# Performance work log

Measured on AMD Instinct MI355X. Metric: run time of the kernel, lower is better.

The kernel has to match this reference:

```python
import jax, jax.numpy as jnp
import numpy as np

CLIP_TEMPERATURE = 1.0


def setup_inputs() -> dict:
    key = jax.random.key(0)
    k1, k2 = jax.random.split(key)
    N, D = 16384, 256
    x = jax.random.normal(k1, (N, D), dtype=jnp.float32)
    y = jax.random.normal(k2, (N, D), dtype=jnp.float32)
    return {"x": x, "y": y}


def reference(x, y):
    # logits[i, j] = <x_i, y_j> / T ; labels are the diagonal (i-th text matches i-th image)
    logits = jnp.einsum('id,jd->ij', x, y) / CLIP_TEMPERATURE  # [N, N]
    N = logits.shape[0]
    diag_idx = jnp.arange(N)
    # CrossEntropy(logits, labels=arange) == -mean(diag(log_softmax(logits, axis=1)))
    lsm_row = jax.nn.log_softmax(logits, axis=1)  # image -> text
    lsm_col = jax.nn.log_softmax(logits, axis=0)  # text  -> image (== log_softmax(logits.T, axis=1).T)
    loss_row = -jnp.mean(lsm_row[diag_idx, diag_idx])
    loss_col = -jnp.mean(lsm_col[diag_idx, diag_idx])
    return (loss_row + loss_col) * 0.5
```

## Files before the change

### kernel.cpp

```cpp
#include <hip/hip_runtime.h>
#include <hip/hip_bf16.h>

#define NN 16384
#define DD 256
#define PANEL 256
#define JCOLS 128
#define BKT 64
#define NT 4
#define NJ 16
#define THREADS 512
#define A_BYTES (PANEL * DD * 2)
#define B_BYTES (JCOLS * BKT * 2)
#define LDS_TOTAL (A_BYTES + 2 * B_BYTES)
#define SHIFT_C 64.0f
#define LOG2E 1.4426950408889634f

typedef __attribute__((ext_vector_type(4))) float f32x4;
typedef __attribute__((ext_vector_type(8))) short bf16x8;

#if __has_builtin(__builtin_amdgcn_exp2f)
#define EXP2F(x) __builtin_amdgcn_exp2f(x)
#else
#define EXP2F(x) exp2f(x)
#endif

__device__ __forceinline__ unsigned pkbf(float a, float b) {
  float2 t; t.x = a; t.y = b;
  __hip_bfloat162 h = __float22bfloat162_rn(t);
  union { __hip_bfloat162 h; unsigned u; } cv;
  cv.h = h;
  return cv.u;
}

__device__ __forceinline__ float rowsum16_dpp(float v) {
  union { float f; int i; } x, t;
  x.f = v;
  t.i = __builtin_amdgcn_update_dpp(0, x.i, 0x111, 0xf, 0xf, true); x.f += t.f;
  t.i = __builtin_amdgcn_update_dpp(0, x.i, 0x112, 0xf, 0xf, true); x.f += t.f;
  t.i = __builtin_amdgcn_update_dpp(0, x.i, 0x114, 0xf, 0xf, true); x.f += t.f;
  t.i = __builtin_amdgcn_update_dpp(0, x.i, 0x118, 0xf, 0xf, true); x.f += t.f;
  return x.f;
}

__global__ __launch_bounds__(256) void cvt_kernel(
    const float* __restrict__ X, const float* __restrict__ Y,
    unsigned short* __restrict__ Xb, unsigned short* __restrict__ Yb) {
  const int groups_per_arr = NN * DD / 8;
  int g = blockIdx.x * 256 + threadIdx.x;
  const float* src;
  unsigned short* dst;
  if (g < groups_per_arr) { src = X; dst = Xb; }
  else { src = Y; dst = Yb; g -= groups_per_arr; }
  float4 a = ((const float4*)src)[(size_t)g * 2];
  float4 b = ((const float4*)src)[(size_t)g * 2 + 1];
  uint4 p = { pkbf(a.x, a.y), pkbf(a.z, a.w), pkbf(b.x, b.y), pkbf(b.z, b.w) };
  ((uint4*)dst)[g] = p;
}

__global__ __launch_bounds__(THREADS, 2) void clip_gemm(
    const unsigned short* __restrict__ Xb, const unsigned short* __restrict__ Yb,
    float* __restrict__ rowsum, float* __restrict__ colsum,
    float* __restrict__ diagsum) {
  extern __shared__ unsigned char sm[];

  const int tid = threadIdx.x;
  const int bid = blockIdx.x;
  const int xcd = bid & 7;
  const int panel = xcd * 8 + ((bid >> 3) & 7);
  const int colgroup = bid >> 6;
  const int rowbase = panel * PANEL;
  const int colbase = colgroup * (NJ * JCOLS);

  const unsigned short* xb = Xb + (size_t)rowbase * DD;
  const unsigned short* ybg = Yb + (size_t)colbase * DD;

  const int wid = tid >> 6, lane = tid & 63;
  const int wm = wid >> 1, wn = wid & 1;
  const int lm = lane & 15, lk = lane >> 4;

#pragma unroll
  for (int p = 0; p < 16; ++p) {
    const int s = p * 512 + tid;
    const int row = s >> 5;
    const int g = (s & 31) ^ (row & 7);
    __builtin_amdgcn_global_load_lds(
        (const __attribute__((address_space(1))) unsigned*)(xb + row * DD + g * 8),
        (__attribute__((address_space(3))) unsigned*)(sm + s * 16), 16, 0, 0);
  }

  int bsrc[2], bdst[2];
#pragma unroll
  for (int p = 0; p < 2; ++p) {
    const int s = p * 512 + tid;
    const int row = s >> 3;
    const int g = (s & 7) ^ (row & 7);
    bsrc[p] = row * DD + g * 8;
    bdst[p] = A_BYTES + s * 16;
  }

#define GLOADB(jn, tn, buf)                                                    \
  {                                                                            \
    _Pragma("unroll")                                                          \
    for (int p = 0; p < 2; ++p)                                                \
      __builtin_amdgcn_global_load_lds(                                        \
          (const __attribute__((address_space(1))) unsigned*)(ybg + (size_t)(jn) * (JCOLS * DD) + bsrc[p] + (tn) * BKT), \
          (__attribute__((address_space(3))) unsigned*)(sm + (buf) * B_BYTES + bdst[p]), \
          16, 0, 0);                                                           \
  }

#define RDA(m, t, kh)                                                          \
  (*(const bf16x8*)(sm + (wm * 64 + (m) * 16 + lm) * (DD * 2) +                \
                    ((((t) * 8 + (kh) * 4 + lk) ^ (lm & 7)) << 4)))
#define RDB(nf, kh, buf)                                                       \
  (*(const bf16x8*)(sm + A_BYTES + (buf) * B_BYTES +                           \
                    (wn * 64 + (nf) * 16 + lm) * (BKT * 2) +                   \
                    ((((kh) * 4 + lk) ^ (lm & 7)) << 4)))

  f32x4 acc[4][4] = {};
  float rowacc[4][4];
#pragma unroll
  for (int m = 0; m < 4; ++m)
#pragma unroll
    for (int r = 0; r < 4; ++r) rowacc[m][r] = 0.f;
  float dsum = 0.f;
  const float negC = -(SHIFT_C * LOG2E);

  GLOADB(0, 0, 0);

  for (int j = 0; j < NJ; ++j) {
#pragma unroll
    for (int t = 0; t < NT; ++t) {
      __syncthreads();
      if (t < NT - 1) { GLOADB(j, t + 1, (t + 1) & 1); }
      else if (j < NJ - 1) { GLOADB(j + 1, 0, 0); }
      const int buf = t & 1;
      bf16x8 a0, b0[4];
#pragma unroll
      for (int kh = 0; kh < 2; ++kh) {
#pragma unroll
        for (int nf = 0; nf < 4; ++nf) b0[nf] = RDB(nf, kh, buf);
#pragma unroll
        for (int m = 0; m < 4; ++m) {
          a0 = RDA(m, t, kh);
#pragma unroll
          for (int nf = 0; nf < 4; ++nf)
            acc[m][nf] = __builtin_amdgcn_mfma_f32_16x16x32_bf16(a0, b0[nf], acc[m][nf], 0, 0, 0);
        }
      }
    }

    const int jc0 = colbase + j * JCOLS;
    float colacc[4] = {0.f, 0.f, 0.f, 0.f};
#pragma unroll
    for (int m = 0; m < 4; ++m)
#pragma unroll
      for (int nf = 0; nf < 4; ++nf)
#pragma unroll
        for (int r = 0; r < 4; ++r) {
          float e = EXP2F(__builtin_fmaf(acc[m][nf][r], LOG2E, negC));
          rowacc[m][r] += e;
          colacc[nf] += e;
        }
    if (jc0 < rowbase + PANEL && jc0 + JCOLS > rowbase) {
#pragma unroll
      for (int m = 0; m < 4; ++m)
#pragma unroll
        for (int nf = 0; nf < 4; ++nf)
#pragma unroll
          for (int r = 0; r < 4; ++r) {
            const int gr = rowbase + wm * 64 + m * 16 + lk * 4 + r;
            const int gc = jc0 + wn * 64 + nf * 16 + lm;
            if (gr == gc) dsum += acc[m][nf][r];
          }
    }
#pragma unroll
    for (int nf = 0; nf < 4; ++nf) {
      float v = colacc[nf];
      v += __shfl_xor(v, 16);
      v += __shfl_xor(v, 32);
      if (lk == 0)
        atomicAdd(&colsum[jc0 + wn * 64 + nf * 16 + lm], v);
    }
    const f32x4 z4 = {0.f, 0.f, 0.f, 0.f};
#pragma unroll
    for (int m = 0; m < 4; ++m)
#pragma unroll
      for (int nf = 0; nf < 4; ++nf) acc[m][nf] = z4;
  }
#undef GLOADB
#undef RDA
#undef RDB

  {
    float d = dsum;
    d += __shfl_xor(d, 1);
    d += __shfl_xor(d, 2);
    d += __shfl_xor(d, 4);
    d += __shfl_xor(d, 8);
    d += __shfl_xor(d, 16);
    d += __shfl_xor(d, 32);
    if (lane == 0 && d != 0.f) atomicAdd(diagsum, d);
  }
#pragma unroll
  for (int m = 0; m < 4; ++m)
#pragma unroll
    for (int r = 0; r < 4; ++r) {
      float v = rowsum16_dpp(rowacc[m][r]);
      if (lm == 15)
        atomicAdd(&rowsum[rowbase + wm * 64 + m * 16 + lk * 4 + r], v);
    }
}

__global__ __launch_bounds__(256) void clip_main_fb(
    const float* __restrict__ X, const float* __restrict__ Y,
    float* __restrict__ rowsum, float* __restrict__ colsum,
    float* __restrict__ diagsum) {
  __shared__ __align__(16) unsigned char smem[2 * 128 * 64 * 2];
  unsigned char* smA = smem;
  unsigned char* smB = smem + 128 * 64 * 2;

  const int tid = threadIdx.x;
  const int bid = blockIdx.x;
  const int swz = (bid & 7) * 2048 + (bid >> 3);
  const int brow = swz >> 7;
  const int bcol = swz & 127;

  const float* xb = X + (size_t)brow * 128 * DD;
  const float* yb = Y + (size_t)bcol * 128 * DD;

  const int wid = tid >> 6, lane = tid & 63;
  const int wm = wid >> 1, wn = wid & 1;
  const int lm = lane & 15, lk = lane >> 4;

  f32x4 acc[4][4] = {};

  for (int ks = 0; ks < 4; ++ks) {
    const int kbase = ks * 64;
    if (ks) __syncthreads();
#pragma unroll
    for (int i = 0; i < 4; ++i) {
      const int c = tid + i * 256;
      const int row = c >> 3, slot = c & 7;
      const int boff = row * 128 + ((slot << 4) ^ ((row & 7) << 4));
      const float* ga = xb + row * DD + kbase + (slot << 3);
      float4 a0 = *(const float4*)ga;
      float4 a1 = *(const float4*)(ga + 4);
      uint4 pa = { pkbf(a0.x, a0.y), pkbf(a0.z, a0.w),
                   pkbf(a1.x, a1.y), pkbf(a1.z, a1.w) };
      *(uint4*)(smA + boff) = pa;
      const float* gb = yb + row * DD + kbase + (slot << 3);
      float4 b0 = *(const float4*)gb;
      float4 b1 = *(const float4*)(gb + 4);
      uint4 pb = { pkbf(b0.x, b0.y), pkbf(b0.z, b0.w),
                   pkbf(b1.x, b1.y), pkbf(b1.z, b1.w) };
      *(uint4*)(smB + boff) = pb;
    }
    __syncthreads();

#pragma unroll
    for (int kk = 0; kk < 2; ++kk) {
      const int kboff = kk * 64 + lk * 16;
      bf16x8 a[4], b[4];
#pragma unroll
      for (int m = 0; m < 4; ++m) {
        const int row = wm * 64 + m * 16 + lm;
        a[m] = *(const bf16x8*)(smA + row * 128 + (kboff ^ ((row & 7) << 4)));
      }
#pragma unroll
      for (int n = 0; n < 4; ++n) {
        const int row = wn * 64 + n * 16 + lm;
        b[n] = *(const bf16x8*)(smB + row * 128 + (kboff ^ ((row & 7) << 4)));
      }
#pragma unroll
      for (int m = 0; m < 4; ++m)
#pragma unroll
        for (int n = 0; n < 4; ++n)
          acc[m][n] = __builtin_amdgcn_mfma_f32_16x16x32_bf16(a[m], b[n], acc[m][n], 0, 0, 0);
    }
  }

  float rowacc[4][4];
  float colacc[4];
#pragma unroll
  for (int m = 0; m < 4; ++m)
#pragma unroll
    for (int r = 0; r < 4; ++r) rowacc[m][r] = 0.f;
#pragma unroll
  for (int n = 0; n < 4; ++n) colacc[n] = 0.f;

  const float negC = -(SHIFT_C * LOG2E);
#pragma unroll
  for (int m = 0; m < 4; ++m)
#pragma unroll
    for (int n = 0; n < 4; ++n)
#pragma unroll
      for (int r = 0; r < 4; ++r) {
        float e = EXP2F(__builtin_fmaf(acc[m][n][r], LOG2E, negC));
        rowacc[m][r] += e;
        colacc[n] += e;
      }

  if (brow == bcol && wm == wn) {
    float dsum = 0.f;
#pragma unroll
    for (int m = 0; m < 4; ++m)
#pragma unroll
      for (int n = 0; n < 4; ++n)
#pragma unroll
        for (int r = 0; r < 4; ++r) {
          const int rr = m * 16 + lk * 4 + r;
          const int cc = n * 16 + lm;
          if (rr == cc) dsum += acc[m][n][r];
        }
    dsum += __shfl_xor(dsum, 1);
    dsum += __shfl_xor(dsum, 2);
    dsum += __shfl_xor(dsum, 4);
    dsum += __shfl_xor(dsum, 8);
    dsum += __shfl_xor(dsum, 16);
    dsum += __shfl_xor(dsum, 32);
    if (lane == 0) atomicAdd(diagsum, dsum);
  }

#pragma unroll
  for (int m = 0; m < 4; ++m)
#pragma unroll
    for (int r = 0; r < 4; ++r) {
      float v = rowsum16_dpp(rowacc[m][r]);
      if (lm == 15)
        atomicAdd(&rowsum[brow * 128 + wm * 64 + m * 16 + lk * 4 + r], v);
    }
#pragma unroll
  for (int n = 0; n < 4; ++n) {
    float v = colacc[n];
    v += __shfl_xor(v, 16);
    v += __shfl_xor(v, 32);
    if (lk == 0)
      atomicAdd(&colsum[bcol * 128 + wn * 64 + n * 16 + lm], v);
  }
}

__global__ __launch_bounds__(256) void clip_stats(
    const float* __restrict__ rowsum, const float* __restrict__ colsum,
    float* __restrict__ partial) {
  __shared__ float sdata[4];
  const int i = blockIdx.x * 256 + threadIdx.x;
  float s = logf(rowsum[i]) + logf(colsum[i]);
  s += __shfl_xor(s, 1);
  s += __shfl_xor(s, 2);
  s += __shfl_xor(s, 4);
  s += __shfl_xor(s, 8);
  s += __shfl_xor(s, 16);
  s += __shfl_xor(s, 32);
  const int lane = threadIdx.x & 63, wv = threadIdx.x >> 6;
  if (lane == 0) sdata[wv] = s;
  __syncthreads();
  if (threadIdx.x == 0)
    atomicAdd(partial, sdata[0] + sdata[1] + sdata[2] + sdata[3]);
}

__global__ void clip_out(const float* __restrict__ partial,
                         const float* __restrict__ diagsum,
                         float* __restrict__ out) {
  if (threadIdx.x == 0)
    out[0] = (float)((double)SHIFT_C + (double)partial[0] * 0.5 / (double)NN
                     - (double)diagsum[0] / (double)NN);
}

extern "C" void kernel_launch(void* const* d_in, const int* in_sizes, int n_in,
                              void* d_out, int out_size, void* d_ws, size_t ws_size,
                              hipStream_t stream) {
  const float* X = (const float*)d_in[0];
  const float* Y = (const float*)d_in[1];

  const size_t bf16_bytes = (size_t)2 * NN * DD * sizeof(unsigned short);
  const size_t stats_bytes = (size_t)(2 * NN + 2) * sizeof(float);

  if (ws_size >= bf16_bytes + stats_bytes) {
    unsigned short* Xb = (unsigned short*)d_ws;
    unsigned short* Yb = Xb + (size_t)NN * DD;
    float* rowsum = (float*)((unsigned char*)d_ws + bf16_bytes);
    float* colsum = rowsum + NN;
    float* diagsum = colsum + NN;
    float* partial = diagsum + 1;

    hipMemsetAsync(rowsum, 0, stats_bytes, stream);
    cvt_kernel<<<dim3(2 * NN * DD / 8 / 256), dim3(256), 0, stream>>>(X, Y, Xb, Yb);
    clip_gemm<<<dim3(512), dim3(THREADS), LDS_TOTAL, stream>>>(
        Xb, Yb, rowsum, colsum, diagsum);
    clip_stats<<<dim3(NN / 256), dim3(256), 0, stream>>>(rowsum, colsum, partial);
    clip_out<<<dim3(1), dim3(64), 0, stream>>>(partial, diagsum, (float*)d_out);
  } else {
    float* rowsum = (float*)d_ws;
    float* colsum = rowsum + NN;
    float* diagsum = colsum + NN;
    float* partial = diagsum + 1;
    hipMemsetAsync(d_ws, 0, stats_bytes, stream);
    clip_main_fb<<<dim3((NN / 128) * (NN / 128)), dim3(256), 0, stream>>>(
        X, Y, rowsum, colsum, diagsum);
    clip_stats<<<dim3(NN / 256), dim3(256), 0, stream>>>(rowsum, colsum, partial);
    clip_out<<<dim3(1), dim3(64), 0, stream>>>(partial, diagsum, (float*)d_out);
  }
}
```

Baseline: 210.2 us.

## Load B operands directly into registers and remap blocks so XCDs share column groups

Drops the LDS double buffer for the Y tile and its per-step __syncthreads; each wave instead fetches its B fragments straight from global memory into registers, prefetched one k-step ahead. Block indexing is also remapped so consecutive blocks (spread across XCDs) take different column groups of the same row panel. The goal is to remove barrier stalls and LDS traffic for B. The cost is redundant global/L2 reads, since the waves that share a column (wm varies) each load the same B data, plus more registers held for the prefetch.

```diff
diff --git a/kernel.cpp b/kernel.cpp
--- a/kernel.cpp
+++ b/kernel.cpp
@@ -5,13 +5,10 @@
 #define DD 256
 #define PANEL 256
 #define JCOLS 128
-#define BKT 64
 #define NT 4
 #define NJ 16
 #define THREADS 512
 #define A_BYTES (PANEL * DD * 2)
-#define B_BYTES (JCOLS * BKT * 2)
-#define LDS_TOTAL (A_BYTES + 2 * B_BYTES)
 #define SHIFT_C 64.0f
 #define LOG2E 1.4426950408889634f
 
@@ -65,9 +62,8 @@
 
   const int tid = threadIdx.x;
   const int bid = blockIdx.x;
-  const int xcd = bid & 7;
-  const int panel = xcd * 8 + ((bid >> 3) & 7);
-  const int colgroup = bid >> 6;
+  const int colgroup = bid & 7;
+  const int panel = bid >> 3;
   const int rowbase = panel * PANEL;
   const int colbase = colgroup * (NJ * JCOLS);
 
@@ -87,34 +83,22 @@
         (const __attribute__((address_space(1))) unsigned*)(xb + row * DD + g * 8),
         (__attribute__((address_space(3))) unsigned*)(sm + s * 16), 16, 0, 0);
   }
-
-  int bsrc[2], bdst[2];
-#pragma unroll
-  for (int p = 0; p < 2; ++p) {
-    const int s = p * 512 + tid;
-    const int row = s >> 3;
-    const int g = (s & 7) ^ (row & 7);
-    bsrc[p] = row * DD + g * 8;
-    bdst[p] = A_BYTES + s * 16;
-  }
-
-#define GLOADB(jn, tn, buf)                                                    \
-  {                                                                            \
-    _Pragma("unroll")                                                          \
-    for (int p = 0; p < 2; ++p)                                                \
-      __builtin_amdgcn_global_load_lds(                                        \
-          (const __attribute__((address_space(1))) unsigned*)(ybg + (size_t)(jn) * (JCOLS * DD) + bsrc[p] + (tn) * BKT), \
-          (__attribute__((address_space(3))) unsigned*)(sm + (buf) * B_BYTES + bdst[p]), \
-          16, 0, 0);                                                           \
-  }
+  __syncthreads();
 
 #define RDA(m, t, kh)                                                          \
   (*(const bf16x8*)(sm + (wm * 64 + (m) * 16 + lm) * (DD * 2) +                \
                     ((((t) * 8 + (kh) * 4 + lk) ^ (lm & 7)) << 4)))
-#define RDB(nf, kh, buf)                                                       \
-  (*(const bf16x8*)(sm + A_BYTES + (buf) * B_BYTES +                           \
-                    (wn * 64 + (nf) * 16 + lm) * (BKT * 2) +                   \
-                    ((((kh) * 4 + lk) ^ (lm & 7)) << 4)))
+
+  const unsigned short* ybl = ybg + (size_t)(wn * 64 + lm) * DD + lk * 8;
+
+#define LOADB(dst, yj, t)                                                      \
+  {                                                                            \
+    _Pragma("unroll")                                                          \
+    for (int nf = 0; nf < 4; ++nf) {                                           \
+      dst[0][nf] = *(const bf16x8*)((yj) + nf * 16 * DD + (t) * 64);           \
+      dst[1][nf] = *(const bf16x8*)((yj) + nf * 16 * DD + (t) * 64 + 32);      \
+    }                                                                          \
+  }
 
   f32x4 acc[4][4] = {};
   float rowacc[4][4];
@@ -125,26 +109,25 @@
   float dsum = 0.f;
   const float negC = -(SHIFT_C * LOG2E);
 
-  GLOADB(0, 0, 0);
+  bf16x8 breg[2][2][4];
+
+  LOADB(breg[0], ybl, 0);
 
   for (int j = 0; j < NJ; ++j) {
+    const unsigned short* yj = ybl + (size_t)j * (JCOLS * DD);
 #pragma unroll
     for (int t = 0; t < NT; ++t) {
-      __syncthreads();
-      if (t < NT - 1) { GLOADB(j, t + 1, (t + 1) & 1); }
-      else if (j < NJ - 1) { GLOADB(j + 1, 0, 0); }
-      const int buf = t & 1;
-      bf16x8 a0, b0[4];
+      if (t < NT - 1) { LOADB(breg[(t + 1) & 1], yj, t + 1); }
+      else if (j < NJ - 1) { LOADB(breg[0], yj + (JCOLS * DD), 0); }
 #pragma unroll
       for (int kh = 0; kh < 2; ++kh) {
 #pragma unroll
-        for (int nf = 0; nf < 4; ++nf) b0[nf] = RDB(nf, kh, buf);
-#pragma unroll
         for (int m = 0; m < 4; ++m) {
-          a0 = RDA(m, t, kh);
+          const bf16x8 a0 = RDA(m, t, kh);
 #pragma unroll
           for (int nf = 0; nf < 4; ++nf)
-            acc[m][nf] = __builtin_amdgcn_mfma_f32_16x16x32_bf16(a0, b0[nf], acc[m][nf], 0, 0, 0);
+            acc[m][nf] = __builtin_amdgcn_mfma_f32_16x16x32_bf16(
+                a0, breg[t & 1][kh][nf], acc[m][nf], 0, 0, 0);
         }
       }
     }
@@ -187,9 +170,8 @@
 #pragma unroll
       for (int nf = 0; nf < 4; ++nf) acc[m][nf] = z4;
   }
-#undef GLOADB
+#undef LOADB
 #undef RDA
-#undef RDB
 
   {
     float d = dsum;
@@ -385,7 +367,7 @@
 
     hipMemsetAsync(rowsum, 0, stats_bytes, stream);
     cvt_kernel<<<dim3(2 * NN * DD / 8 / 256), dim3(256), 0, stream>>>(X, Y, Xb, Yb);
-    clip_gemm<<<dim3(512), dim3(THREADS), LDS_TOTAL, stream>>>(
+    clip_gemm<<<dim3(512), dim3(THREADS), A_BYTES, stream>>>(
         Xb, Yb, rowsum, colsum, diagsum);
     clip_stats<<<dim3(NN / 256), dim3(256), 0, stream>>>(rowsum, colsum, partial);
     clip_out<<<dim3(1), dim3(64), 0, stream>>>(partial, diagsum, (float*)d_out);
```

Result: slower. 386.8 us (+84.0%).

## Shrink GEMM tiles to 128-row panels with 256 threads and static LDS

Applied to the files above, without the earlier changes.

Each block now handles 128 rows instead of 256, using 4 waves instead of 8. The B k-step drops from 64 to 32, so there are 8 k-tiles with a matching swizzle. The grid doubles to 1024 blocks with a simpler panel/column-group mapping that drops the XCD-aware assignment, and LDS becomes a static 80KB array so more blocks can be resident per CU. The cost is half the X-panel reuse, twice as many reads of Y across panels, and more barriers per output tile.

```diff
diff --git a/kernel.cpp b/kernel.cpp
--- a/kernel.cpp
+++ b/kernel.cpp
@@ -3,15 +3,14 @@
 
 #define NN 16384
 #define DD 256
-#define PANEL 256
+#define PANEL 128
 #define JCOLS 128
-#define BKT 64
-#define NT 4
+#define BK 32
+#define NT 8
 #define NJ 16
-#define THREADS 512
+#define THREADS 256
 #define A_BYTES (PANEL * DD * 2)
-#define B_BYTES (JCOLS * BKT * 2)
-#define LDS_TOTAL (A_BYTES + 2 * B_BYTES)
+#define B_BYTES (JCOLS * BK * 2)
 #define SHIFT_C 64.0f
 #define LOG2E 1.4426950408889634f
 
@@ -61,13 +60,12 @@
     const unsigned short* __restrict__ Xb, const unsigned short* __restrict__ Yb,
     float* __restrict__ rowsum, float* __restrict__ colsum,
     float* __restrict__ diagsum) {
-  extern __shared__ unsigned char sm[];
+  __shared__ __align__(16) unsigned char sm[A_BYTES + 2 * B_BYTES];
 
   const int tid = threadIdx.x;
   const int bid = blockIdx.x;
-  const int xcd = bid & 7;
-  const int panel = xcd * 8 + ((bid >> 3) & 7);
-  const int colgroup = bid >> 6;
+  const int colgroup = bid & 7;
+  const int panel = bid >> 3;
   const int rowbase = panel * PANEL;
   const int colbase = colgroup * (NJ * JCOLS);
 
@@ -80,7 +78,7 @@
 
 #pragma unroll
   for (int p = 0; p < 16; ++p) {
-    const int s = p * 512 + tid;
+    const int s = p * 256 + tid;
     const int row = s >> 5;
     const int g = (s & 31) ^ (row & 7);
     __builtin_amdgcn_global_load_lds(
@@ -91,10 +89,10 @@
   int bsrc[2], bdst[2];
 #pragma unroll
   for (int p = 0; p < 2; ++p) {
-    const int s = p * 512 + tid;
-    const int row = s >> 3;
-    const int g = (s & 7) ^ (row & 7);
-    bsrc[p] = row * DD + g * 8;
+    const int s = p * 256 + tid;
+    const int col = s >> 2;
+    const int g = (s & 3) ^ (col & 3);
+    bsrc[p] = col * DD + g * 8;
     bdst[p] = A_BYTES + s * 16;
   }
 
@@ -103,18 +101,18 @@
     _Pragma("unroll")                                                          \
     for (int p = 0; p < 2; ++p)                                                \
       __builtin_amdgcn_global_load_lds(                                        \
-          (const __attribute__((address_space(1))) unsigned*)(ybg + (size_t)(jn) * (JCOLS * DD) + bsrc[p] + (tn) * BKT), \
+          (const __attribute__((address_space(1))) unsigned*)(ybg + (size_t)(jn) * (JCOLS * DD) + bsrc[p] + (tn) * BK), \
           (__attribute__((address_space(3))) unsigned*)(sm + (buf) * B_BYTES + bdst[p]), \
           16, 0, 0);                                                           \
   }
 
-#define RDA(m, t, kh)                                                          \
+#define RDA(m, t)                                                              \
   (*(const bf16x8*)(sm + (wm * 64 + (m) * 16 + lm) * (DD * 2) +                \
-                    ((((t) * 8 + (kh) * 4 + lk) ^ (lm & 7)) << 4)))
-#define RDB(nf, kh, buf)                                                       \
+                    ((((t) * 4 + lk) ^ (lm & 7)) << 4)))
+#define RDB(nf, buf)                                                           \
   (*(const bf16x8*)(sm + A_BYTES + (buf) * B_BYTES +                           \
-                    (wn * 64 + (nf) * 16 + lm) * (BKT * 2) +                   \
-                    ((((kh) * 4 + lk) ^ (lm & 7)) << 4)))
+                    (wn * 64 + (nf) * 16 + lm) * (BK * 2) +                    \
+                    ((lk ^ (lm & 3)) << 4)))
 
   f32x4 acc[4][4] = {};
   float rowacc[4][4];
@@ -134,18 +132,15 @@
       if (t < NT - 1) { GLOADB(j, t + 1, (t + 1) & 1); }
       else if (j < NJ - 1) { GLOADB(j + 1, 0, 0); }
       const int buf = t & 1;
-      bf16x8 a0, b0[4];
-#pragma unroll
-      for (int kh = 0; kh < 2; ++kh) {
-#pragma unroll
-        for (int nf = 0; nf < 4; ++nf) b0[nf] = RDB(nf, kh, buf);
-#pragma unroll
-        for (int m = 0; m < 4; ++m) {
-          a0 = RDA(m, t, kh);
-#pragma unroll
-          for (int nf = 0; nf < 4; ++nf)
-            acc[m][nf] = __builtin_amdgcn_mfma_f32_16x16x32_bf16(a0, b0[nf], acc[m][nf], 0, 0, 0);
-        }
+      bf16x8 b0[4];
+#pragma unroll
+      for (int nf = 0; nf < 4; ++nf) b0[nf] = RDB(nf, buf);
+#pragma unroll
+      for (int m = 0; m < 4; ++m) {
+        const bf16x8 a0 = RDA(m, t);
+#pragma unroll
+        for (int nf = 0; nf < 4; ++nf)
+          acc[m][nf] = __builtin_amdgcn_mfma_f32_16x16x32_bf16(a0, b0[nf], acc[m][nf], 0, 0, 0);
       }
     }
 
@@ -161,16 +156,16 @@
           rowacc[m][r] += e;
           colacc[nf] += e;
         }
-    if (jc0 < rowbase + PANEL && jc0 + JCOLS > rowbase) {
+    if (jc0 == rowbase) {
 #pragma unroll
       for (int m = 0; m < 4; ++m)
 #pragma unroll
         for (int nf = 0; nf < 4; ++nf)
 #pragma unroll
           for (int r = 0; r < 4; ++r) {
-            const int gr = rowbase + wm * 64 + m * 16 + lk * 4 + r;
-            const int gc = jc0 + wn * 64 + nf * 16 + lm;
-            if (gr == gc) dsum += acc[m][nf][r];
+            const int rr = wm * 64 + m * 16 + lk * 4 + r;
+            const int cc = wn * 64 + nf * 16 + lm;
+            if (rr == cc) dsum += acc[m][nf][r];
           }
     }
 #pragma unroll
@@ -385,7 +380,7 @@
 
     hipMemsetAsync(rowsum, 0, stats_bytes, stream);
     cvt_kernel<<<dim3(2 * NN * DD / 8 / 256), dim3(256), 0, stream>>>(X, Y, Xb, Yb);
-    clip_gemm<<<dim3(512), dim3(THREADS), LDS_TOTAL, stream>>>(
+    clip_gemm<<<dim3((NN / PANEL) * 8), dim3(THREADS), 0, stream>>>(
         Xb, Yb, rowsum, colsum, diagsum);
     clip_stats<<<dim3(NN / 256), dim3(256), 0, stream>>>(rowsum, colsum, partial);
     clip_out<<<dim3(1), dim3(64), 0, stream>>>(partial, diagsum, (float*)d_out);
```

After: 194.1 us. 7.7% less time.
